# Optimization experiments

Hardware: AMD Instinct MI355X
Metric: run time of the kernel (lower is better)

The kernel has to match this reference:

```python
import jax, jax.numpy as jnp
import numpy as np

B, M, T, H = 32, 2048, 8, 64  # batch, measurements, num_tags, hidden_dim
LATENT, TRIL = 3, 6
NEG_INF = -1e9  # masked-out logit value for segment softmax


def _linear_init(key, fan_in, fan_out):
    # torch nn.Linear default: U(-1/sqrt(fan_in), 1/sqrt(fan_in)) for W and b
    bound = 1.0 / np.sqrt(fan_in)
    kw, kb = jax.random.split(key)
    w = jax.random.uniform(kw, (fan_in, fan_out), minval=-bound, maxval=bound, dtype=jnp.float32)
    b = jax.random.uniform(kb, (fan_out,), minval=-bound, maxval=bound, dtype=jnp.float32)
    return w, b


def setup_inputs() -> dict:
    key = jax.random.key(0)
    ks = jax.random.split(key, 14)
    inp = {}
    inp['measurements'] = jax.random.normal(ks[0], (B, M, 5), dtype=jnp.float32)
    inp['measurement_to_tag_mapping'] = jax.random.randint(ks[1], (B, M), 0, T, dtype=jnp.int32)
    inp['me_w1'], inp['me_b1'] = _linear_init(ks[2], 5, H)
    inp['me_w2'], inp['me_b2'] = _linear_init(ks[3], H, H)
    inp['q_w'], inp['q_b'] = _linear_init(ks[4], H, H)
    inp['k_w'], inp['k_b'] = _linear_init(ks[5], H, H)
    inp['v_w'], inp['v_b'] = _linear_init(ks[6], H, H)
    inp['a1_w1'], inp['a1_b1'] = _linear_init(ks[7], H, H // 2)
    inp['a1_w2'], inp['a1_b2'] = _linear_init(ks[8], H // 2, 1)
    inp['a2_w1'], inp['a2_b1'] = _linear_init(ks[9], H, H // 2)
    inp['a2_w2'], inp['a2_b2'] = _linear_init(ks[10], H // 2, 1)
    inp['mu_w'], inp['mu_b'] = _linear_init(ks[11], H, LATENT)
    inp['logL_w'], inp['logL_b'] = _linear_init(ks[12], H, TRIL)
    return inp


def reference(measurements, measurement_to_tag_mapping,
              me_w1, me_b1, me_w2, me_b2,
              q_w, q_b, k_w, k_b, v_w, v_b,
              a1_w1, a1_b1, a1_w2, a1_b2,
              a2_w1, a2_b1, a2_w2, a2_b2,
              mu_w, mu_b, logL_w, logL_b):
    # measurement encoder: two Linear+ReLU layers -> [B, M, H]
    feat = jax.nn.relu(measurements @ me_w1 + me_b1)
    feat = jax.nn.relu(feat @ me_w2 + me_b2)

    # self-attention with residual
    q = feat @ q_w + q_b
    k = feat @ k_w + k_b
    v = feat @ v_w + v_b
    scale = jnp.sqrt(jnp.float32(H))
    scores = jnp.einsum('bmh,bnh->bmn', q, k) / scale  # [B, M, M]
    feat = feat + jnp.einsum('bmn,bnh->bmh', jax.nn.softmax(scores, axis=-1), v)

    # per-measurement attention logits (attention_net1) -> [B, M]
    a1 = (jax.nn.relu(feat @ a1_w1 + a1_b1) @ a1_w2 + a1_b2)[..., 0]

    # segment softmax per tag id: mask [B, M, T]
    tag_mask = measurement_to_tag_mapping[..., None] == jnp.arange(T)
    seg_logits = jnp.where(tag_mask, a1[..., None], NEG_INF)
    seg_w = jax.nn.softmax(seg_logits, axis=1)  # softmax over measurements within each tag
    tag_feat = jnp.einsum('bmt,bmh->bth', seg_w, feat)  # [B, T, H]

    # aggregate tags (attention_net2) -> pose feature [B, H]
    a2 = (jax.nn.relu(tag_feat @ a2_w1 + a2_b1) @ a2_w2 + a2_b2)[..., 0]  # [B, T]
    tag_w = jax.nn.softmax(a2, axis=-1)
    pose = jnp.einsum('bt,bth->bh', tag_w, tag_feat)

    mu = pose @ mu_w + mu_b
    logL = pose @ logL_w + logL_b
    return mu, logL
```

## Files before the change

### kernel.cpp

```cpp
#include <hip/hip_runtime.h>
#include <hip/hip_bf16.h>
#include <cstdint>
#include <cstddef>


typedef short s16x8 __attribute__((ext_vector_type(8)));
typedef float f32x4 __attribute__((ext_vector_type(4)));
typedef float f32x16 __attribute__((ext_vector_type(16)));

#define LOG2E  1.4426950408889634f
#define QSCALE 0.18033688011112042f

__device__ __forceinline__ unsigned short f2bf(float f) {
    unsigned u = __builtin_bit_cast(unsigned, f);
    u += 0x7fffu + ((u >> 16) & 1u);
    return (unsigned short)(u >> 16);
}

__device__ __forceinline__ unsigned cvtpk(float lo, float hi) {
    unsigned r;
    asm("v_cvt_pk_bf16_f32 %0, %1, %2" : "=v"(r) : "v"(lo), "v"(hi));
    return r;
}

__device__ __forceinline__ float exp2_raw(float x) {
    float r;
    asm("v_exp_f32 %0, %1" : "=v"(r) : "v"(x));
    return r;
}

#define PLSWAP(a, b) asm("v_permlane32_swap_b32 %0, %1" : "+v"(a), "+v"(b))

#define WAITBAR(N) do { \
    asm volatile("s_waitcnt vmcnt(" #N ")\n\ts_barrier" ::: "memory"); \
    __builtin_amdgcn_sched_barrier(0); \
} while (0)

__device__ __forceinline__ void gload_lds16(const void* g, void* l) {
    __builtin_amdgcn_global_load_lds((const __attribute__((address_space(1))) void*)g,
                                     (__attribute__((address_space(3))) void*)l, 16, 0, 0);
}

#define MFMA16(a, b, c) __builtin_amdgcn_mfma_f32_16x16x32_bf16((a), (b), (c), 0, 0, 0)
#define MFMA32(a, b, c) __builtin_amdgcn_mfma_f32_32x32x16_bf16((a), (b), (c), 0, 0, 0)

__global__ void k_prep(const float* __restrict__ w2, const float* __restrict__ qw,
                       const float* __restrict__ kw, const float* __restrict__ vw,
                       unsigned short* __restrict__ wt)
{
    int tid = blockIdx.x * 256 + threadIdx.x;
    for (int idx = tid; idx < 4096; idx += 2048) {
        int o = idx >> 6, i = idx & 63;
        wt[idx]         = f2bf(w2[i * 64 + o]);
        wt[4096 + idx]  = f2bf(qw[i * 64 + o] * QSCALE);
        wt[8192 + idx]  = f2bf(kw[i * 64 + o]);
        wt[12288 + idx] = f2bf(vw[i * 64 + o]);
    }
}

__global__ __launch_bounds__(256)
void k_encode(const float* __restrict__ meas, const float* __restrict__ w1,
              const float* __restrict__ b1, const float* __restrict__ b2,
              const float* __restrict__ qb, const float* __restrict__ kb,
              const float* __restrict__ vb,
              const unsigned short* __restrict__ wt,
              float* __restrict__ feat,
              unsigned short* __restrict__ qbf, unsigned short* __restrict__ kbf,
              unsigned short* __restrict__ vt)
{
    __shared__ __align__(16) unsigned short hbuf[4][1152];
    int tid = threadIdx.x;
    int w = tid >> 6, lane = tid & 63;
    int g = lane >> 4, c16 = lane & 15;
    int m0 = (blockIdx.x * 4 + w) * 16;
    int b  = m0 >> 11;
    unsigned short* hb = hbuf[w];
    int vrow = lane >> 2, vseg = lane & 3;

    float x[5];
    const float* xr = meas + (size_t)(m0 + c16) * 5;
#pragma unroll
    for (int i = 0; i < 5; ++i) x[i] = xr[i];
    s16x8 aH[2];
#pragma unroll
    for (int s = 0; s < 2; ++s) {
#pragma unroll
        for (int jj = 0; jj < 8; ++jj) {
            int j = 8 * g + jj + 32 * s;
            float acc = b1[j];
#pragma unroll
            for (int i = 0; i < 5; ++i) acc += x[i] * w1[i * 64 + j];
            aH[s][jj] = (short)f2bf(fmaxf(acc, 0.f));
        }
    }

    const f32x4 zero = {0.f, 0.f, 0.f, 0.f};
    f32x4 c[4];

#pragma unroll
    for (int dt = 0; dt < 4; ++dt) {
        c[dt] = zero;
#pragma unroll
        for (int s = 0; s < 2; ++s) {
            s16x8 bf = *(const s16x8*)(wt + (c16 + 16 * dt) * 64 + 32 * s + 8 * g);
            c[dt] = MFMA16(aH[s], bf, c[dt]);
        }
    }
#pragma unroll
    for (int dt = 0; dt < 4; ++dt) {
        int d = c16 + 16 * dt;
        float bias = b2[d];
#pragma unroll
        for (int r = 0; r < 4; ++r) {
            float v = fmaxf(c[dt][r] + bias, 0.f);
            feat[(size_t)(m0 + 4 * g + r) * 64 + d] = v;
            hb[(4 * g + r) * 72 + d] = f2bf(v);
        }
    }
    s16x8 aF[2];
#pragma unroll
    for (int s = 0; s < 2; ++s)
        aF[s] = *(const s16x8*)(hb + c16 * 72 + 32 * s + 8 * g);

    auto gemmW = [&](const unsigned short* wmat, f32x4* cc) {
#pragma unroll
        for (int dt = 0; dt < 4; ++dt) {
            cc[dt] = zero;
#pragma unroll
            for (int s = 0; s < 2; ++s) {
                s16x8 bf = *(const s16x8*)(wmat + (c16 + 16 * dt) * 64 + 32 * s + 8 * g);
                cc[dt] = MFMA16(aF[s], bf, cc[dt]);
            }
        }
    };
    auto storeV = [&](const float* bias4, unsigned short* dstbase) {
#pragma unroll
        for (int dt = 0; dt < 4; ++dt) {
            int d = c16 + 16 * dt;
#pragma unroll
            for (int r = 0; r < 4; ++r)
                hb[(4 * g + r) * 72 + d] = f2bf(c[dt][r] + bias4[dt]);
        }
        s16x8 o0 = *(const s16x8*)(hb + vrow * 72 + vseg * 16);
        s16x8 o1 = *(const s16x8*)(hb + vrow * 72 + vseg * 16 + 8);
        unsigned short* dst = dstbase + (size_t)(m0 + vrow) * 64 + vseg * 16;
        *(s16x8*)dst = o0;
        *(s16x8*)(dst + 8) = o1;
    };

    float bias4[4];
    gemmW(wt + 4096, c);
#pragma unroll
    for (int dt = 0; dt < 4; ++dt) bias4[dt] = qb[c16 + 16 * dt] * QSCALE;
    storeV(bias4, qbf);
    gemmW(wt + 8192, c);
#pragma unroll
    for (int dt = 0; dt < 4; ++dt) bias4[dt] = kb[c16 + 16 * dt];
    storeV(bias4, kbf);
    gemmW(wt + 12288, c);
#pragma unroll
    for (int dt = 0; dt < 4; ++dt) {
        int d = c16 + 16 * dt;
        float bias = vb[d];
#pragma unroll
        for (int r = 0; r < 4; ++r)
            hb[(4 * g + r) * 72 + d] = f2bf(c[dt][r] + bias);
    }
    unsigned short tvv[16];
#pragma unroll
    for (int mr = 0; mr < 16; ++mr) tvv[mr] = hb[mr * 72 + lane];
    s16x8 v0, v1;
#pragma unroll
    for (int e2 = 0; e2 < 8; ++e2) { v0[e2] = (short)tvv[e2]; v1[e2] = (short)tvv[8 + e2]; }
    unsigned short* dst = vt + ((size_t)b * 64 + lane) * 2048 + (m0 & 2047);
    *(s16x8*)dst = v0;
    *(s16x8*)(dst + 8) = v1;
}

__global__ __launch_bounds__(512, 4)
void k_attn(const unsigned short* __restrict__ qbf, const unsigned short* __restrict__ kbf,
            const unsigned short* __restrict__ vt, float* __restrict__ feat)
{
    __shared__ __align__(16) char smem[49152];

    int tid = threadIdx.x;
    int w_ = tid >> 6, lane = tid & 63;
    int h = lane >> 5, c32 = lane & 31;
    int jhalf = w_ & 1, tile = w_ >> 1;
    int bid = (int)blockIdx.x;
    bid = (bid & 7) * 64 + (bid >> 3);
    int b = bid >> 4;
    int q0g = (bid & 15) * 128 + tile * 32;
    size_t rowbase = (size_t)b * 2048;

    const unsigned short* kbf_b = kbf + rowbase * 64;
    const unsigned short* vt_b  = vt + (size_t)b * 64 * 2048;

    s16x8 qf[4];
    {
        const unsigned short* qp = qbf + (rowbase + q0g + c32) * 64 + 8 * h;
#pragma unroll
        for (int st = 0; st < 4; ++st)
            qf[st] = *(const s16x8*)(qp + 16 * st);
    }

    f32x16 zero16;
#pragma unroll
    for (int i = 0; i < 16; ++i) zero16[i] = 0.f;

    f32x16 o[2];
#pragma unroll
    for (int dt = 0; dt < 2; ++dt)
#pragma unroll
        for (int i = 0; i < 16; ++i) o[dt][i] = 0.f;
    float ll = 0.f;

    int srow = 8 * w_ + (lane >> 3);
    int scol = (lane & 7) ^ (srow & 7);
    const unsigned short* gk0 = kbf_b + (size_t)srow * 64 + scol * 8;
    const unsigned short* gv0 = vt_b + (size_t)srow * 2048 + scol * 8;

    auto stage = [&](int kt, int buf) {
        gload_lds16(gk0 + (size_t)kt * 4096, smem + buf * 8192 + w_ * 1024);
        gload_lds16(gv0 + kt * 64, smem + 24576 + buf * 8192 + w_ * 1024);
    };

    int swz = c32 & 7;
    int krow = 32 * jhalf + c32;

    auto compute = [&](int buf) {
        const char* Kb = smem + buf * 8192;
        const char* Vb = smem + 24576 + buf * 8192;

        s16x8 kf[4], vf[2][2];
#pragma unroll
        for (int st = 0; st < 4; ++st)
            kf[st] = *(const s16x8*)(Kb + krow * 128 + (((2 * st + h) ^ swz) * 16));
#pragma unroll
        for (int ks = 0; ks < 2; ++ks)
#pragma unroll
            for (int dt = 0; dt < 2; ++dt)
                vf[ks][dt] = *(const s16x8*)(Vb + (32 * dt + c32) * 128 +
                                             (((4 * jhalf + 2 * ks + h) ^ swz) * 16));

        __builtin_amdgcn_s_setprio(1);
        f32x16 sc = MFMA32(kf[0], qf[0], zero16);
#pragma unroll
        for (int st = 1; st < 4; ++st)
            sc = MFMA32(kf[st], qf[st], sc);
        __builtin_amdgcn_s_setprio(0);

        float p[16];
#pragma unroll
        for (int i = 0; i < 16; ++i) p[i] = exp2_raw(sc[i]);

        float s;
        {
            float a0 = p[0] + p[1],  a1 = p[2] + p[3],  a2 = p[4] + p[5],  a3 = p[6] + p[7];
            float a4 = p[8] + p[9],  a5 = p[10] + p[11], a6 = p[12] + p[13], a7 = p[14] + p[15];
            float b0 = a0 + a1, b1 = a2 + a3, b2 = a4 + a5, b3 = a6 + a7;
            s = (b0 + b1) + (b2 + b3);
        }
        {
            float s1 = s, s2 = s;
            PLSWAP(s1, s2);
            s = s1 + s2;
        }
        ll += s;

        unsigned u[8];
#pragma unroll
        for (int k2 = 0; k2 < 8; ++k2) u[k2] = cvtpk(p[2 * k2], p[2 * k2 + 1]);

        __builtin_amdgcn_s_setprio(1);
#pragma unroll
        for (int ks = 0; ks < 2; ++ks) {
            unsigned a0 = u[4 * ks + 0], b0 = u[4 * ks + 2];
            unsigned a1 = u[4 * ks + 1], b1 = u[4 * ks + 3];
            PLSWAP(a0, b0);
            PLSWAP(a1, b1);
            union { unsigned uu[4]; s16x8 v; } pa;
            pa.uu[0] = a0; pa.uu[1] = a1; pa.uu[2] = b0; pa.uu[3] = b1;
#pragma unroll
            for (int dt = 0; dt < 2; ++dt)
                o[dt] = MFMA32(pa.v, vf[ks][dt], o[dt]);
        }
        __builtin_amdgcn_s_setprio(0);
    };

    stage(0, 0);
    stage(1, 1);
    WAITBAR(2);

#pragma unroll 3
    for (int kt = 0; kt < 30; ++kt) {
        stage(kt + 2, (kt + 2) % 3);
        compute(kt % 3);
        WAITBAR(2);
    }
    compute(0);
    WAITBAR(0);
    compute(1);
    __syncthreads();

    float* Om = (float*)smem;
    float* Ml = (float*)(smem + 36864);
    if (jhalf) {
#pragma unroll
        for (int dt = 0; dt < 2; ++dt)
#pragma unroll
            for (int rg = 0; rg < 4; ++rg) {
                f32x4 vv;
#pragma unroll
                for (int r = 0; r < 4; ++r) vv[r] = o[dt][4 * rg + r];
                *(f32x4*)&Om[(tile * 64 + 32 * dt + c32) * 36 + 8 * rg + 4 * h] = vv;
            }
        if (h == 0) Ml[tile * 32 + c32] = ll;
    }
    __syncthreads();
    if (!jhalf) {
        float l1 = Ml[tile * 32 + c32];
        float f = 1.f / (ll + l1);
        float fr[16];
#pragma unroll
        for (int r = 0; r < 16; ++r) {
            int qrow = (r & 3) + 8 * (r >> 2) + 4 * h;
            fr[r] = __shfl(f, qrow);
        }
#pragma unroll
        for (int dt = 0; dt < 2; ++dt)
#pragma unroll
            for (int rg = 0; rg < 4; ++rg) {
                f32x4 pv = *(const f32x4*)&Om[(tile * 64 + 32 * dt + c32) * 36 + 8 * rg + 4 * h];
#pragma unroll
                for (int r = 0; r < 4; ++r) {
                    int rr = 4 * rg + r;
                    int qrow = r + 8 * rg + 4 * h;
                    size_t fi = (rowbase + q0g + qrow) * 64 + 32 * dt + c32;
                    feat[fi] += (o[dt][rr] + pv[r]) * fr[rr];
                }
            }
    }
}

__global__ __launch_bounds__(256)
void k_a1tag(const float* __restrict__ feat, const int* __restrict__ map,
             const float* __restrict__ a1w1, const float* __restrict__ b1,
             const float* __restrict__ w2, const float* __restrict__ b2,
             float* __restrict__ part1, float* __restrict__ part0)
{
    __shared__ float psum[128][33];
    __shared__ float es[128];
    __shared__ float accv[4][8][64];
    __shared__ float s0red[4][8];

    int b = blockIdx.x >> 4;
    int c = blockIdx.x & 15;
    int tid = threadIdx.x, lane = tid & 63, w = tid >> 6;
    int m0 = c * 128;
    const int* mp = map + b * 2048 + m0;
    const float* fbase = feat + ((size_t)b * 2048 + m0) * 64;

    {
        int r = tid & 127, kh = tid >> 7;
        const f32x4* fr4 = (const f32x4*)(fbase + (size_t)r * 64 + kh * 32);
        float acc[32];
#pragma unroll
        for (int j = 0; j < 32; ++j) acc[j] = kh ? 0.f : b1[j];
#pragma unroll
        for (int kc = 0; kc < 8; ++kc) {
            f32x4 fv = fr4[kc];
#pragma unroll
            for (int ki = 0; ki < 4; ++ki) {
                const float* wr = a1w1 + (kh * 32 + kc * 4 + ki) * 32;
#pragma unroll
                for (int j = 0; j < 32; ++j)
                    acc[j] = fmaf(fv[ki], wr[j], acc[j]);
            }
        }
        if (kh) {
#pragma unroll
            for (int j = 0; j < 32; ++j) psum[r][j] = acc[j];
        }
        __syncthreads();
        if (!kh) {
            float s = b2[0];
#pragma unroll
            for (int j = 0; j < 32; ++j)
                s += fmaxf(acc[j] + psum[r][j], 0.f) * w2[j];
            es[r] = exp2_raw(s * LOG2E);
        }
    }
    __syncthreads();

    float tacc[8], s0t[8];
#pragma unroll
    for (int t = 0; t < 8; ++t) { tacc[t] = 0.f; s0t[t] = 0.f; }
    for (int mi = w; mi < 128; mi += 4) {
        int tg = mp[mi];
        float e = es[mi];
        float wf = e * fbase[(size_t)mi * 64 + lane];
#pragma unroll
        for (int t = 0; t < 8; ++t)
            if (tg == t) { tacc[t] += wf; s0t[t] += e; }
    }
#pragma unroll
    for (int t = 0; t < 8; ++t) accv[w][t][lane] = tacc[t];
    if (lane == 0) {
#pragma unroll
        for (int t = 0; t < 8; ++t) s0red[w][t] = s0t[t];
    }
    __syncthreads();
    for (int e = tid; e < 512; e += 256) {
        int t = e >> 6, d = e & 63;
        part1[((size_t)c * 32 + b) * 512 + e] =
            accv[0][t][d] + accv[1][t][d] + accv[2][t][d] + accv[3][t][d];
    }
    if (tid < 8)
        part0[((size_t)c * 32 + b) * 8 + tid] =
            s0red[0][tid] + s0red[1][tid] + s0red[2][tid] + s0red[3][tid];
}

__global__ __launch_bounds__(256)
void k_head(const float* __restrict__ part1, const float* __restrict__ part0,
            const float* __restrict__ a2w1, const float* __restrict__ a2b1,
            const float* __restrict__ a2w2, const float* __restrict__ a2b2,
            const float* __restrict__ muw, const float* __restrict__ mub,
            const float* __restrict__ lLw, const float* __restrict__ lLb,
            float* __restrict__ out)
{
    __shared__ float tf[8][64];
    __shared__ float deni[8];
    __shared__ float sc8[8];
    __shared__ float pose[64];
    int b = blockIdx.x;
    int tid = threadIdx.x;

    if (tid < 8) {
        float s = 0.f;
#pragma unroll
        for (int c = 0; c < 16; ++c) s += part0[((size_t)c * 32 + b) * 8 + tid];
        deni[tid] = 1.f / s;
    }
    __syncthreads();
    for (int e = tid; e < 512; e += 256) {
        float s = 0.f;
#pragma unroll
        for (int c = 0; c < 16; ++c) s += part1[((size_t)c * 32 + b) * 512 + e];
        tf[e >> 6][e & 63] = s * deni[e >> 6];
    }
    __syncthreads();

    {
        int t = tid >> 5, j = tid & 31;
        float acc = a2b1[j];
        for (int d = 0; d < 64; ++d) acc += tf[t][d] * a2w1[d * 32 + j];
        float hsum = fmaxf(acc, 0.f) * a2w2[j];
        hsum += __shfl_xor(hsum, 1);
        hsum += __shfl_xor(hsum, 2);
        hsum += __shfl_xor(hsum, 4);
        hsum += __shfl_xor(hsum, 8);
        hsum += __shfl_xor(hsum, 16);
        if (j == 0) sc8[t] = hsum + a2b2[0];
    }
    __syncthreads();
    if (tid < 64) {
        float smax = sc8[0];
#pragma unroll
        for (int t = 1; t < 8; ++t) smax = fmaxf(smax, sc8[t]);
        float e[8], ssum = 0.f;
#pragma unroll
        for (int t = 0; t < 8; ++t) { e[t] = exp2f((sc8[t] - smax) * LOG2E); ssum += e[t]; }
        float rinv = 1.f / ssum;
        float p = 0.f;
#pragma unroll
        for (int t = 0; t < 8; ++t) p += (e[t] * rinv) * tf[t][tid];
        pose[tid] = p;
    }
    __syncthreads();
    if (tid < 3) {
        float acc = mub[tid];
        for (int d = 0; d < 64; ++d) acc += pose[d] * muw[d * 3 + tid];
        out[b * 3 + tid] = acc;
    }
    if (tid >= 32 && tid < 38) {
        int oo = tid - 32;
        float acc = lLb[oo];
        for (int d = 0; d < 64; ++d) acc += pose[d] * lLw[d * 6 + oo];
        out[96 + b * 6 + oo] = acc;
    }
}

extern "C" void kernel_launch(void* const* d_in, const int* in_sizes, int n_in,
                              void* d_out, int out_size, void* d_ws, size_t ws_size,
                              hipStream_t stream)
{
    (void)in_sizes; (void)n_in; (void)out_size; (void)ws_size;

    const float* measurements = (const float*)d_in[0];
    const int*   mapping      = (const int*)d_in[1];
    const float* me_w1 = (const float*)d_in[2];
    const float* me_b1 = (const float*)d_in[3];
    const float* me_w2 = (const float*)d_in[4];
    const float* me_b2 = (const float*)d_in[5];
    const float* q_w   = (const float*)d_in[6];
    const float* q_b   = (const float*)d_in[7];
    const float* k_w   = (const float*)d_in[8];
    const float* k_b   = (const float*)d_in[9];
    const float* v_w   = (const float*)d_in[10];
    const float* v_b   = (const float*)d_in[11];
    const float* a1_w1 = (const float*)d_in[12];
    const float* a1_b1 = (const float*)d_in[13];
    const float* a1_w2 = (const float*)d_in[14];
    const float* a1_b2 = (const float*)d_in[15];
    const float* a2_w1 = (const float*)d_in[16];
    const float* a2_b1 = (const float*)d_in[17];
    const float* a2_w2 = (const float*)d_in[18];
    const float* a2_b2 = (const float*)d_in[19];
    const float* mu_w  = (const float*)d_in[20];
    const float* mu_b  = (const float*)d_in[21];
    const float* logL_w = (const float*)d_in[22];
    const float* logL_b = (const float*)d_in[23];

    char* ws = (char*)d_ws;
    unsigned short* wt    = (unsigned short*)(ws);
    float*          feat  = (float*)(ws + 40960);
    unsigned short* qbf   = (unsigned short*)(ws + 16818176);
    unsigned short* kbf   = (unsigned short*)(ws + 25206784);
    unsigned short* vt    = (unsigned short*)(ws + 33595392);
    float*          part1 = (float*)(ws + 42248192);
    float*          part0 = (float*)(ws + 43296768);
    float*          out   = (float*)d_out;

    k_prep<<<8, 256, 0, stream>>>(me_w2, q_w, k_w, v_w, wt);
    k_encode<<<1024, 256, 0, stream>>>(measurements, me_w1, me_b1, me_b2, q_b, k_b, v_b,
                                       wt, feat, qbf, kbf, vt);
    k_attn<<<512, 512, 0, stream>>>(qbf, kbf, vt, feat);
    k_a1tag<<<512, 256, 0, stream>>>(feat, mapping, a1_w1, a1_b1, a1_w2, a1_b2,
                                     part1, part0);
    k_head<<<32, 256, 0, stream>>>(part1, part0, a2_w1, a2_b1, a2_w2, a2_b2,
                                   mu_w, mu_b, logL_w, logL_b, out);
}
```

Baseline: 111.6 us.

## Process two query tiles per wave in attention to reuse K/V fragments

Halves the attention block to 256 threads and has each wave handle two 32-row query tiles, so the K and V fragments read from LDS are reused across both tiles. Each thread now issues four global-to-LDS loads per stage instead of two, and the wait counts are adjusted to match. The aim is to cut LDS read traffic per MFMA. The cost is more registers per wave (two accumulator sets and two Q fragment sets) and half as many waves to hide latency.

```diff
diff --git a/kernel.cpp b/kernel.cpp
--- a/kernel.cpp
+++ b/kernel.cpp
@@ -177,7 +177,7 @@
     *(s16x8*)(dst + 8) = v1;
 }
 
-__global__ __launch_bounds__(512, 4)
+__global__ __launch_bounds__(256, 2)
 void k_attn(const unsigned short* __restrict__ qbf, const unsigned short* __restrict__ kbf,
             const unsigned short* __restrict__ vt, float* __restrict__ feat)
 {
@@ -186,43 +186,51 @@
     int tid = threadIdx.x;
     int w_ = tid >> 6, lane = tid & 63;
     int h = lane >> 5, c32 = lane & 31;
-    int jhalf = w_ & 1, tile = w_ >> 1;
+    int jhalf = w_ & 1, tpair = w_ >> 1;
     int bid = (int)blockIdx.x;
     bid = (bid & 7) * 64 + (bid >> 3);
     int b = bid >> 4;
-    int q0g = (bid & 15) * 128 + tile * 32;
+    int q0g = (bid & 15) * 128;
     size_t rowbase = (size_t)b * 2048;
 
     const unsigned short* kbf_b = kbf + rowbase * 64;
     const unsigned short* vt_b  = vt + (size_t)b * 64 * 2048;
 
-    s16x8 qf[4];
-    {
-        const unsigned short* qp = qbf + (rowbase + q0g + c32) * 64 + 8 * h;
+    s16x8 qf[2][4];
+#pragma unroll
+    for (int ti = 0; ti < 2; ++ti) {
+        const unsigned short* qp =
+            qbf + (rowbase + q0g + (2 * tpair + ti) * 32 + c32) * 64 + 8 * h;
 #pragma unroll
         for (int st = 0; st < 4; ++st)
-            qf[st] = *(const s16x8*)(qp + 16 * st);
+            qf[ti][st] = *(const s16x8*)(qp + 16 * st);
     }
 
     f32x16 zero16;
 #pragma unroll
     for (int i = 0; i < 16; ++i) zero16[i] = 0.f;
 
-    f32x16 o[2];
+    f32x16 oA[2], oB[2];
 #pragma unroll
     for (int dt = 0; dt < 2; ++dt)
 #pragma unroll
-        for (int i = 0; i < 16; ++i) o[dt][i] = 0.f;
-    float ll = 0.f;
-
-    int srow = 8 * w_ + (lane >> 3);
-    int scol = (lane & 7) ^ (srow & 7);
-    const unsigned short* gk0 = kbf_b + (size_t)srow * 64 + scol * 8;
-    const unsigned short* gv0 = vt_b + (size_t)srow * 2048 + scol * 8;
+        for (int i = 0; i < 16; ++i) { oA[dt][i] = 0.f; oB[dt][i] = 0.f; }
+    float llA = 0.f, llB = 0.f;
+
+    int r0 = tid >> 3,         g0 = (tid & 7) ^ (r0 & 7);
+    int r1 = (tid + 256) >> 3, g1 = (tid & 7) ^ (r1 & 7);
+    const unsigned short* gkA = kbf_b + r0 * 64 + g0 * 8;
+    const unsigned short* gkB = kbf_b + r1 * 64 + g1 * 8;
+    const unsigned short* gvA = vt_b + (size_t)r0 * 2048 + g0 * 8;
+    const unsigned short* gvB = vt_b + (size_t)r1 * 2048 + g1 * 8;
 
     auto stage = [&](int kt, int buf) {
-        gload_lds16(gk0 + (size_t)kt * 4096, smem + buf * 8192 + w_ * 1024);
-        gload_lds16(gv0 + kt * 64, smem + 24576 + buf * 8192 + w_ * 1024);
+        char* kd = smem + buf * 8192 + w_ * 1024;
+        char* vd = smem + 24576 + buf * 8192 + w_ * 1024;
+        gload_lds16(gkA + (size_t)kt * 4096, kd);
+        gload_lds16(gkB + (size_t)kt * 4096, kd + 4096);
+        gload_lds16(gvA + kt * 64, vd);
+        gload_lds16(gvB + kt * 64, vd + 4096);
     };
 
     int swz = c32 & 7;
@@ -243,60 +251,66 @@
                 vf[ks][dt] = *(const s16x8*)(Vb + (32 * dt + c32) * 128 +
                                              (((4 * jhalf + 2 * ks + h) ^ swz) * 16));
 
-        __builtin_amdgcn_s_setprio(1);
-        f32x16 sc = MFMA32(kf[0], qf[0], zero16);
-#pragma unroll
-        for (int st = 1; st < 4; ++st)
-            sc = MFMA32(kf[st], qf[st], sc);
-        __builtin_amdgcn_s_setprio(0);
-
-        float p[16];
-#pragma unroll
-        for (int i = 0; i < 16; ++i) p[i] = exp2_raw(sc[i]);
-
-        float s;
-        {
-            float a0 = p[0] + p[1],  a1 = p[2] + p[3],  a2 = p[4] + p[5],  a3 = p[6] + p[7];
-            float a4 = p[8] + p[9],  a5 = p[10] + p[11], a6 = p[12] + p[13], a7 = p[14] + p[15];
-            float b0 = a0 + a1, b1 = a2 + a3, b2 = a4 + a5, b3 = a6 + a7;
-            s = (b0 + b1) + (b2 + b3);
-        }
-        {
-            float s1 = s, s2 = s;
-            PLSWAP(s1, s2);
-            s = s1 + s2;
-        }
-        ll += s;
-
-        unsigned u[8];
-#pragma unroll
-        for (int k2 = 0; k2 < 8; ++k2) u[k2] = cvtpk(p[2 * k2], p[2 * k2 + 1]);
-
-        __builtin_amdgcn_s_setprio(1);
-#pragma unroll
-        for (int ks = 0; ks < 2; ++ks) {
-            unsigned a0 = u[4 * ks + 0], b0 = u[4 * ks + 2];
-            unsigned a1 = u[4 * ks + 1], b1 = u[4 * ks + 3];
-            PLSWAP(a0, b0);
-            PLSWAP(a1, b1);
-            union { unsigned uu[4]; s16x8 v; } pa;
-            pa.uu[0] = a0; pa.uu[1] = a1; pa.uu[2] = b0; pa.uu[3] = b1;
-#pragma unroll
-            for (int dt = 0; dt < 2; ++dt)
-                o[dt] = MFMA32(pa.v, vf[ks][dt], o[dt]);
-        }
-        __builtin_amdgcn_s_setprio(0);
+#pragma unroll
+        for (int ti = 0; ti < 2; ++ti) {
+            f32x16* o = ti ? oB : oA;
+            float& ll = ti ? llB : llA;
+
+            __builtin_amdgcn_s_setprio(1);
+            f32x16 sc = MFMA32(kf[0], qf[ti][0], zero16);
+#pragma unroll
+            for (int st = 1; st < 4; ++st)
+                sc = MFMA32(kf[st], qf[ti][st], sc);
+            __builtin_amdgcn_s_setprio(0);
+
+            float p[16];
+#pragma unroll
+            for (int i = 0; i < 16; ++i) p[i] = exp2_raw(sc[i]);
+
+            float s;
+            {
+                float a0 = p[0] + p[1],  a1 = p[2] + p[3],  a2 = p[4] + p[5],  a3 = p[6] + p[7];
+                float a4 = p[8] + p[9],  a5 = p[10] + p[11], a6 = p[12] + p[13], a7 = p[14] + p[15];
+                float b0 = a0 + a1, b1 = a2 + a3, b2 = a4 + a5, b3 = a6 + a7;
+                s = (b0 + b1) + (b2 + b3);
+            }
+            {
+                float s1 = s, s2 = s;
+                PLSWAP(s1, s2);
+                s = s1 + s2;
+            }
+            ll += s;
+
+            unsigned u[8];
+#pragma unroll
+            for (int k2 = 0; k2 < 8; ++k2) u[k2] = cvtpk(p[2 * k2], p[2 * k2 + 1]);
+
+            __builtin_amdgcn_s_setprio(1);
+#pragma unroll
+            for (int ks = 0; ks < 2; ++ks) {
+                unsigned a0 = u[4 * ks + 0], b0 = u[4 * ks + 2];
+                unsigned a1 = u[4 * ks + 1], b1 = u[4 * ks + 3];
+                PLSWAP(a0, b0);
+                PLSWAP(a1, b1);
+                union { unsigned uu[4]; s16x8 v; } pa;
+                pa.uu[0] = a0; pa.uu[1] = a1; pa.uu[2] = b0; pa.uu[3] = b1;
+#pragma unroll
+                for (int dt = 0; dt < 2; ++dt)
+                    o[dt] = MFMA32(pa.v, vf[ks][dt], o[dt]);
+            }
+            __builtin_amdgcn_s_setprio(0);
+        }
     };
 
     stage(0, 0);
     stage(1, 1);
-    WAITBAR(2);
+    WAITBAR(4);
 
 #pragma unroll 3
     for (int kt = 0; kt < 30; ++kt) {
         stage(kt + 2, (kt + 2) % 3);
         compute(kt % 3);
-        WAITBAR(2);
+        WAITBAR(4);
     }
     compute(0);
     WAITBAR(0);
@@ -307,39 +321,50 @@
     float* Ml = (float*)(smem + 36864);
     if (jhalf) {
 #pragma unroll
-        for (int dt = 0; dt < 2; ++dt)
-#pragma unroll
-            for (int rg = 0; rg < 4; ++rg) {
-                f32x4 vv;
-#pragma unroll
-                for (int r = 0; r < 4; ++r) vv[r] = o[dt][4 * rg + r];
-                *(f32x4*)&Om[(tile * 64 + 32 * dt + c32) * 36 + 8 * rg + 4 * h] = vv;
+        for (int ti = 0; ti < 2; ++ti) {
+            int tg = 2 * tpair + ti;
+            const f32x16* o = ti ? oB : oA;
+#pragma unroll
+            for (int dt = 0; dt < 2; ++dt)
+#pragma unroll
+                for (int rg = 0; rg < 4; ++rg) {
+                    f32x4 vv;
+#pragma unroll
+                    for (int r = 0; r < 4; ++r) vv[r] = o[dt][4 * rg + r];
+                    *(f32x4*)&Om[(tg * 64 + 32 * dt + c32) * 36 + 8 * rg + 4 * h] = vv;
+                }
+            if (h == 0) Ml[tg * 32 + c32] = ti ? llB : llA;
+        }
+    }
+    __syncthreads();
+    if (!jhalf) {
+#pragma unroll
+        for (int ti = 0; ti < 2; ++ti) {
+            int tg = 2 * tpair + ti;
+            const f32x16* o = ti ? oB : oA;
+            float ll = ti ? llB : llA;
+            float l1 = Ml[tg * 32 + c32];
+            float f = 1.f / (ll + l1);
+            float fr[16];
+#pragma unroll
+            for (int r = 0; r < 16; ++r) {
+                int qrow = (r & 3) + 8 * (r >> 2) + 4 * h;
+                fr[r] = __shfl(f, qrow);
             }
-        if (h == 0) Ml[tile * 32 + c32] = ll;
-    }
-    __syncthreads();
-    if (!jhalf) {
-        float l1 = Ml[tile * 32 + c32];
-        float f = 1.f / (ll + l1);
-        float fr[16];
-#pragma unroll
-        for (int r = 0; r < 16; ++r) {
-            int qrow = (r & 3) + 8 * (r >> 2) + 4 * h;
-            fr[r] = __shfl(f, qrow);
-        }
-#pragma unroll
-        for (int dt = 0; dt < 2; ++dt)
-#pragma unroll
-            for (int rg = 0; rg < 4; ++rg) {
-                f32x4 pv = *(const f32x4*)&Om[(tile * 64 + 32 * dt + c32) * 36 + 8 * rg + 4 * h];
-#pragma unroll
-                for (int r = 0; r < 4; ++r) {
-                    int rr = 4 * rg + r;
-                    int qrow = r + 8 * rg + 4 * h;
-                    size_t fi = (rowbase + q0g + qrow) * 64 + 32 * dt + c32;
-                    feat[fi] += (o[dt][rr] + pv[r]) * fr[rr];
+#pragma unroll
+            for (int dt = 0; dt < 2; ++dt)
+#pragma unroll
+                for (int rg = 0; rg < 4; ++rg) {
+                    f32x4 pv = *(const f32x4*)&Om[(tg * 64 + 32 * dt + c32) * 36 + 8 * rg + 4 * h];
+#pragma unroll
+                    for (int r = 0; r < 4; ++r) {
+                        int rr = 4 * rg + r;
+                        int qrow = r + 8 * rg + 4 * h;
+                        size_t fi = (rowbase + q0g + tg * 32 + qrow) * 64 + 32 * dt + c32;
+                        feat[fi] += (o[dt][rr] + pv[r]) * fr[rr];
+                    }
                 }
-            }
+        }
     }
 }
 
@@ -535,7 +560,7 @@
     k_prep<<<8, 256, 0, stream>>>(me_w2, q_w, k_w, v_w, wt);
     k_encode<<<1024, 256, 0, stream>>>(measurements, me_w1, me_b1, me_b2, q_b, k_b, v_b,
                                        wt, feat, qbf, kbf, vt);
-    k_attn<<<512, 512, 0, stream>>>(qbf, kbf, vt, feat);
+    k_attn<<<512, 256, 0, stream>>>(qbf, kbf, vt, feat);
     k_a1tag<<<512, 256, 0, stream>>>(feat, mapping, a1_w1, a1_b1, a1_w2, a1_b2,
                                      part1, part0);
     k_head<<<32, 256, 0, stream>>>(part1, part0, a2_w1, a2_b1, a2_w2, a2_b2,
```

Result: no change. 110.9 us (-0.6%).

## Fuse attention-net1 and per-tag segment reduction into attention kernel epilogue

Applied to the files above, without the earlier changes.

The k_a1tag kernel is removed and its work moves into the k_attn epilogue. The residual-updated features for each 128-row chunk are kept in shared memory instead of being written to global feat and read back. The epilogue then runs the a1 MLP, the exponentials and the per-tag weighted partial sums straight from LDS. This saves one kernel launch and a full global round trip of feat. In exchange, shared memory grows (which can hurt occupancy at 4 blocks per CU), more syncs are added, and the serial epilogue gets longer.

```diff
diff --git a/kernel.cpp b/kernel.cpp
--- a/kernel.cpp
+++ b/kernel.cpp
@@ -179,9 +179,13 @@
 
 __global__ __launch_bounds__(512, 4)
 void k_attn(const unsigned short* __restrict__ qbf, const unsigned short* __restrict__ kbf,
-            const unsigned short* __restrict__ vt, float* __restrict__ feat)
+            const unsigned short* __restrict__ vt, const float* __restrict__ feat,
+            const int* __restrict__ map,
+            const float* __restrict__ a1w1, const float* __restrict__ a1b1,
+            const float* __restrict__ a1w2, const float* __restrict__ a1b2,
+            float* __restrict__ part1, float* __restrict__ part0)
 {
-    __shared__ __align__(16) char smem[49152];
+    __shared__ __align__(16) char smem[52480];
 
     int tid = threadIdx.x;
     int w_ = tid >> 6, lane = tid & 63;
@@ -190,7 +194,8 @@
     int bid = (int)blockIdx.x;
     bid = (bid & 7) * 64 + (bid >> 3);
     int b = bid >> 4;
-    int q0g = (bid & 15) * 128 + tile * 32;
+    int chunk = bid & 15;
+    int q0g = chunk * 128 + tile * 32;
     size_t rowbase = (size_t)b * 2048;
 
     const unsigned short* kbf_b = kbf + rowbase * 64;
@@ -303,18 +308,22 @@
     compute(1);
     __syncthreads();
 
-    float* Om = (float*)smem;
-    float* Ml = (float*)(smem + 36864);
+    float* fls = (float*)smem;
+    float* Ml  = (float*)(smem + 34816);
+    float* es  = (float*)(smem + 35328);
+    float* accv = (float*)(smem + 35840);
+    float* s0r  = (float*)(smem + 52224);
+
     if (jhalf) {
 #pragma unroll
         for (int dt = 0; dt < 2; ++dt)
 #pragma unroll
-            for (int rg = 0; rg < 4; ++rg) {
-                f32x4 vv;
-#pragma unroll
-                for (int r = 0; r < 4; ++r) vv[r] = o[dt][4 * rg + r];
-                *(f32x4*)&Om[(tile * 64 + 32 * dt + c32) * 36 + 8 * rg + 4 * h] = vv;
-            }
+            for (int rg = 0; rg < 4; ++rg)
+#pragma unroll
+                for (int r = 0; r < 4; ++r) {
+                    int row = tile * 32 + r + 8 * rg + 4 * h;
+                    fls[row * 68 + 32 * dt + c32] = o[dt][4 * rg + r];
+                }
         if (h == 0) Ml[tile * 32 + c32] = ll;
     }
     __syncthreads();
@@ -330,95 +339,80 @@
 #pragma unroll
         for (int dt = 0; dt < 2; ++dt)
 #pragma unroll
-            for (int rg = 0; rg < 4; ++rg) {
-                f32x4 pv = *(const f32x4*)&Om[(tile * 64 + 32 * dt + c32) * 36 + 8 * rg + 4 * h];
+            for (int rg = 0; rg < 4; ++rg)
 #pragma unroll
                 for (int r = 0; r < 4; ++r) {
                     int rr = 4 * rg + r;
-                    int qrow = r + 8 * rg + 4 * h;
-                    size_t fi = (rowbase + q0g + qrow) * 64 + 32 * dt + c32;
-                    feat[fi] += (o[dt][rr] + pv[r]) * fr[rr];
+                    int row = tile * 32 + r + 8 * rg + 4 * h;
+                    size_t fi = (rowbase + chunk * 128 + row) * 64 + 32 * dt + c32;
+                    float val = (o[dt][rr] + fls[row * 68 + 32 * dt + c32]) * fr[rr]
+                              + feat[fi];
+                    fls[row * 68 + 32 * dt + c32] = val;
                 }
+    }
+    __syncthreads();
+
+    {
+        int row = tid >> 2, jq = tid & 3;
+        const float* frw = &fls[row * 68];
+        float acc[8];
+#pragma unroll
+        for (int j8 = 0; j8 < 8; ++j8) acc[j8] = 0.f;
+#pragma unroll
+        for (int kc = 0; kc < 16; ++kc) {
+            f32x4 fv = *(const f32x4*)&frw[kc * 4];
+#pragma unroll
+            for (int ki = 0; ki < 4; ++ki) {
+                const float* wr = a1w1 + (kc * 4 + ki) * 32 + jq * 8;
+#pragma unroll
+                for (int j8 = 0; j8 < 8; ++j8)
+                    acc[j8] = fmaf(fv[ki], wr[j8], acc[j8]);
             }
-    }
-}
-
-__global__ __launch_bounds__(256)
-void k_a1tag(const float* __restrict__ feat, const int* __restrict__ map,
-             const float* __restrict__ a1w1, const float* __restrict__ b1,
-             const float* __restrict__ w2, const float* __restrict__ b2,
-             float* __restrict__ part1, float* __restrict__ part0)
-{
-    __shared__ float psum[128][33];
-    __shared__ float es[128];
-    __shared__ float accv[4][8][64];
-    __shared__ float s0red[4][8];
-
-    int b = blockIdx.x >> 4;
-    int c = blockIdx.x & 15;
-    int tid = threadIdx.x, lane = tid & 63, w = tid >> 6;
-    int m0 = c * 128;
-    const int* mp = map + b * 2048 + m0;
-    const float* fbase = feat + ((size_t)b * 2048 + m0) * 64;
+        }
+        float s = 0.f;
+#pragma unroll
+        for (int j8 = 0; j8 < 8; ++j8)
+            s += fmaxf(acc[j8] + a1b1[jq * 8 + j8], 0.f) * a1w2[jq * 8 + j8];
+        s += __shfl_xor(s, 1);
+        s += __shfl_xor(s, 2);
+        if (jq == 0) es[row] = exp2_raw((s + a1b2[0]) * LOG2E);
+    }
+    __syncthreads();
 
     {
-        int r = tid & 127, kh = tid >> 7;
-        const f32x4* fr4 = (const f32x4*)(fbase + (size_t)r * 64 + kh * 32);
-        float acc[32];
-#pragma unroll
-        for (int j = 0; j < 32; ++j) acc[j] = kh ? 0.f : b1[j];
-#pragma unroll
-        for (int kc = 0; kc < 8; ++kc) {
-            f32x4 fv = fr4[kc];
-#pragma unroll
-            for (int ki = 0; ki < 4; ++ki) {
-                const float* wr = a1w1 + (kh * 32 + kc * 4 + ki) * 32;
-#pragma unroll
-                for (int j = 0; j < 32; ++j)
-                    acc[j] = fmaf(fv[ki], wr[j], acc[j]);
-            }
-        }
-        if (kh) {
-#pragma unroll
-            for (int j = 0; j < 32; ++j) psum[r][j] = acc[j];
-        }
-        __syncthreads();
-        if (!kh) {
-            float s = b2[0];
-#pragma unroll
-            for (int j = 0; j < 32; ++j)
-                s += fmaxf(acc[j] + psum[r][j], 0.f) * w2[j];
-            es[r] = exp2_raw(s * LOG2E);
-        }
-    }
-    __syncthreads();
-
-    float tacc[8], s0t[8];
-#pragma unroll
-    for (int t = 0; t < 8; ++t) { tacc[t] = 0.f; s0t[t] = 0.f; }
-    for (int mi = w; mi < 128; mi += 4) {
-        int tg = mp[mi];
-        float e = es[mi];
-        float wf = e * fbase[(size_t)mi * 64 + lane];
-#pragma unroll
-        for (int t = 0; t < 8; ++t)
-            if (tg == t) { tacc[t] += wf; s0t[t] += e; }
-    }
-#pragma unroll
-    for (int t = 0; t < 8; ++t) accv[w][t][lane] = tacc[t];
-    if (lane == 0) {
-#pragma unroll
-        for (int t = 0; t < 8; ++t) s0red[w][t] = s0t[t];
-    }
-    __syncthreads();
-    for (int e = tid; e < 512; e += 256) {
-        int t = e >> 6, d = e & 63;
-        part1[((size_t)c * 32 + b) * 512 + e] =
-            accv[0][t][d] + accv[1][t][d] + accv[2][t][d] + accv[3][t][d];
-    }
-    if (tid < 8)
-        part0[((size_t)c * 32 + b) * 8 + tid] =
-            s0red[0][tid] + s0red[1][tid] + s0red[2][tid] + s0red[3][tid];
+        const int* mp = map + b * 2048 + chunk * 128;
+        float tacc[8], s0t[8];
+#pragma unroll
+        for (int t = 0; t < 8; ++t) { tacc[t] = 0.f; s0t[t] = 0.f; }
+        for (int mi = w_; mi < 128; mi += 8) {
+            int tg = mp[mi];
+            float e = es[mi];
+            float wf = e * fls[mi * 68 + lane];
+#pragma unroll
+            for (int t = 0; t < 8; ++t)
+                if (tg == t) { tacc[t] += wf; s0t[t] += e; }
+        }
+#pragma unroll
+        for (int t = 0; t < 8; ++t) accv[(w_ * 8 + t) * 64 + lane] = tacc[t];
+        if (lane == 0) {
+#pragma unroll
+            for (int t = 0; t < 8; ++t) s0r[w_ * 8 + t] = s0t[t];
+        }
+    }
+    __syncthreads();
+    {
+        int e = tid;
+        float sum = 0.f;
+#pragma unroll
+        for (int w8 = 0; w8 < 8; ++w8) sum += accv[w8 * 512 + e];
+        part1[((size_t)chunk * 32 + b) * 512 + e] = sum;
+        if (tid < 8) {
+            float s = 0.f;
+#pragma unroll
+            for (int w8 = 0; w8 < 8; ++w8) s += s0r[w8 * 8 + tid];
+            part0[((size_t)chunk * 32 + b) * 8 + tid] = s;
+        }
+    }
 }
 
 __global__ __launch_bounds__(256)
@@ -535,9 +529,8 @@
     k_prep<<<8, 256, 0, stream>>>(me_w2, q_w, k_w, v_w, wt);
     k_encode<<<1024, 256, 0, stream>>>(measurements, me_w1, me_b1, me_b2, q_b, k_b, v_b,
                                        wt, feat, qbf, kbf, vt);
-    k_attn<<<512, 512, 0, stream>>>(qbf, kbf, vt, feat);
-    k_a1tag<<<512, 256, 0, stream>>>(feat, mapping, a1_w1, a1_b1, a1_w2, a1_b2,
-                                     part1, part0);
+    k_attn<<<512, 512, 0, stream>>>(qbf, kbf, vt, feat, mapping,
+                                    a1_w1, a1_b1, a1_w2, a1_b2, part1, part0);
     k_head<<<32, 256, 0, stream>>>(part1, part0, a2_w1, a2_b1, a2_w2, a2_b2,
                                    mu_w, mu_b, logL_w, logL_b, out);
 }
```

Result: faster. 108.8 us (-2.4%).
